# Kernel optimization log

Measured on AMD Instinct MI355X. Metric: run time of the kernel, lower is better.

Reference implementation:

```python
import jax, jax.numpy as jnp
import numpy as np
import math

D_MODEL = 512
NUM_HEADS = 8
D_HEAD = D_MODEL // NUM_HEADS
B, S = 8, 1024


def _rel_shift(pos_score):
    # pos_score: [B, H, S, S] -> Transformer-XL relative shift
    b, h, s1, s2 = pos_score.shape
    padded = jnp.concatenate([jnp.zeros((b, h, s1, 1), pos_score.dtype), pos_score], axis=-1)
    padded = padded.reshape(b, h, s2 + 1, s1)
    return padded[:, :, 1:].reshape(b, h, s1, s2)


def setup_inputs() -> dict:
    key = jax.random.key(0)
    ks = jax.random.split(key, 16)
    scale = 1.0 / math.sqrt(D_MODEL)
    inp = {
        'query': jax.random.normal(ks[0], (B, S, D_MODEL), jnp.float32),
        'key': jax.random.normal(ks[1], (B, S, D_MODEL), jnp.float32),
        'value': jax.random.normal(ks[2], (B, S, D_MODEL), jnp.float32),
        'position_emb': jax.random.normal(ks[3], (B, S, D_MODEL), jnp.float32),
        'Wq': jax.random.normal(ks[4], (D_MODEL, D_MODEL), jnp.float32) * scale,
        'bq': jnp.zeros((D_MODEL,), jnp.float32),
        'Wk': jax.random.normal(ks[5], (D_MODEL, D_MODEL), jnp.float32) * scale,
        'bk': jnp.zeros((D_MODEL,), jnp.float32),
        'Wv': jax.random.normal(ks[6], (D_MODEL, D_MODEL), jnp.float32) * scale,
        'bv': jnp.zeros((D_MODEL,), jnp.float32),
        'Wp': jax.random.normal(ks[7], (D_MODEL, D_MODEL), jnp.float32) * scale,
        'u_bias': jax.random.normal(ks[8], (NUM_HEADS, D_HEAD), jnp.float32) * 0.1,
        'v_bias': jax.random.normal(ks[9], (NUM_HEADS, D_HEAD), jnp.float32) * 0.1,
        'Wo': jax.random.normal(ks[10], (D_MODEL, D_MODEL), jnp.float32) * scale,
        'bo': jnp.zeros((D_MODEL,), jnp.float32),
    }
    return inp


def reference(query, key, value, position_emb, Wq, bq, Wk, bk, Wv, bv, Wp, u_bias, v_bias, Wo, bo):
    b, s, _ = query.shape
    q = (query @ Wq + bq).reshape(b, s, NUM_HEADS, D_HEAD)       # [B,S,H,Dh]
    k = (key @ Wk + bk).reshape(b, s, NUM_HEADS, D_HEAD)
    v = (value @ Wv + bv).reshape(b, s, NUM_HEADS, D_HEAD)
    p = (position_emb @ Wp).reshape(b, s, NUM_HEADS, D_HEAD)
    # content score: (q + u) k^T ; pos score: (q + v) p^T with relative shift
    content_score = jnp.einsum('bqhd,bkhd->bhqk', q + u_bias, k)
    pos_score = _rel_shift(jnp.einsum('bqhd,bkhd->bhqk', q + v_bias, p))
    score = (content_score + pos_score) / math.sqrt(D_MODEL)
    atten = jax.nn.softmax(score, axis=-1)                        # dropout off (eval)
    context = jnp.einsum('bhqk,bkhd->bqhd', atten, v).reshape(b, s, D_MODEL)
    return context @ Wo + bo
```

## Files before the change

### kernel.cpp

```cpp
#include <hip/hip_runtime.h>
#include <cstdint>

typedef unsigned short ushort_t;
typedef __attribute__((ext_vector_type(8))) short bf16x8;
typedef __attribute__((ext_vector_type(4))) float f32x4;

#define S_LEN 1024
#define DHEAD 64

__device__ inline ushort_t f2bf(float f) {
    union { float f; uint32_t u; } c; c.f = f;
    uint32_t u = c.u;
    uint32_t r = u + 0x7FFFu + ((u >> 16) & 1u);
    return (ushort_t)(r >> 16);
}
__device__ inline float bf2f(ushort_t h) {
    union { uint32_t u; float f; } c; c.u = ((uint32_t)h) << 16;
    return c.f;
}
__device__ inline bf16x8 load8(const ushort_t* p) {
    union { uint4 u; bf16x8 v; } c;
    c.u = *reinterpret_cast<const uint4*>(p);
    return c.v;
}

__global__ __launch_bounds__(256) void prep_kernel(
    const float* __restrict__ wq, const float* __restrict__ wk,
    const float* __restrict__ wv, const float* __restrict__ wp,
    const float* __restrict__ wo, ushort_t* __restrict__ ws) {
    __shared__ float tile[64][65];
    int wi = blockIdx.z;
    const float* src = wi == 0 ? wq : wi == 1 ? wk : wi == 2 ? wv : wi == 3 ? wp : wo;
    int cx = blockIdx.x * 64;
    int ry = blockIdx.y * 64;
    int t = threadIdx.x;
    int tr = t >> 4;
    int tc = (t & 15) * 4;
#pragma unroll
    for (int i = 0; i < 4; i++) {
        int r = tr + i * 16;
        float4 f = *reinterpret_cast<const float4*>(src + (size_t)(ry + r) * 512 + cx + tc);
        tile[r][tc] = f.x; tile[r][tc + 1] = f.y; tile[r][tc + 2] = f.z; tile[r][tc + 3] = f.w;
    }
    __syncthreads();
    ushort_t* dst = ws + (size_t)wi * 262144;
#pragma unroll
    for (int i = 0; i < 4; i++) {
        int r = tr + i * 16;
        ushort4 o;
        o.x = f2bf(tile[tc][r]); o.y = f2bf(tile[tc + 1][r]);
        o.z = f2bf(tile[tc + 2][r]); o.w = f2bf(tile[tc + 3][r]);
        *reinterpret_cast<ushort4*>(dst + (size_t)(cx + r) * 512 + ry + tc) = o;
    }
}

__global__ __launch_bounds__(256) void proj_gemm(
    const float* __restrict__ qa, const float* __restrict__ ka,
    const float* __restrict__ va, const float* __restrict__ pa,
    const ushort_t* __restrict__ wT,
    const float* __restrict__ bq, const float* __restrict__ bk,
    const float* __restrict__ bv,
    const float* __restrict__ ub, const float* __restrict__ vb,
    ushort_t* __restrict__ Qu, ushort_t* __restrict__ Qv,
    ushort_t* __restrict__ Kp, ushort_t* __restrict__ Pp,
    ushort_t* __restrict__ Vt) {
    __shared__ ushort_t smem[2][128][72];
    int z = blockIdx.z;
    const float* A = z == 0 ? qa : z == 1 ? ka : z == 2 ? pa : va;
    const ushort_t* Bt = wT + (z == 0 ? 0 : z == 1 ? 262144 : z == 2 ? 786432 : 524288);
    const float* bias = z == 0 ? bq : z == 1 ? bk : z == 3 ? bv : nullptr;

    int tid = threadIdx.x;
    int wid = tid >> 6, lane = tid & 63, quad = lane >> 4, l16 = lane & 15;
    int wr = wid >> 1, wc = wid & 1;
    int row0 = blockIdx.y * 128, col0 = blockIdx.x * 128;

    f32x4 acc[4][4];
#pragma unroll
    for (int i = 0; i < 4; i++)
#pragma unroll
        for (int j = 0; j < 4; j++) acc[i][j] = (f32x4){0.f, 0.f, 0.f, 0.f};

    for (int k0 = 0; k0 < 512; k0 += 64) {
#pragma unroll
        for (int i = 0; i < 4; i++) {
            int cid = tid + i * 256;
            int r = cid >> 3, c8 = cid & 7;
            const float* ap = A + (size_t)(row0 + r) * 512 + k0 + c8 * 8;
            float4 f0 = *reinterpret_cast<const float4*>(ap);
            float4 f1 = *reinterpret_cast<const float4*>(ap + 4);
            union { ushort_t s[8]; uint4 u; } pk;
            pk.s[0] = f2bf(f0.x); pk.s[1] = f2bf(f0.y); pk.s[2] = f2bf(f0.z); pk.s[3] = f2bf(f0.w);
            pk.s[4] = f2bf(f1.x); pk.s[5] = f2bf(f1.y); pk.s[6] = f2bf(f1.z); pk.s[7] = f2bf(f1.w);
            *reinterpret_cast<uint4*>(&smem[0][r][c8 * 8]) = pk.u;
            *reinterpret_cast<uint4*>(&smem[1][r][c8 * 8]) =
                *reinterpret_cast<const uint4*>(Bt + (size_t)(col0 + r) * 512 + k0 + c8 * 8);
        }
        __syncthreads();
#pragma unroll
        for (int kc = 0; kc < 2; kc++) {
            bf16x8 af[4], bg[4];
#pragma unroll
            for (int m = 0; m < 4; m++)
                af[m] = load8(&smem[0][wr * 64 + m * 16 + l16][kc * 32 + quad * 8]);
#pragma unroll
            for (int n = 0; n < 4; n++)
                bg[n] = load8(&smem[1][wc * 64 + n * 16 + l16][kc * 32 + quad * 8]);
#pragma unroll
            for (int m = 0; m < 4; m++)
#pragma unroll
                for (int n = 0; n < 4; n++)
                    acc[m][n] = __builtin_amdgcn_mfma_f32_16x16x32_bf16(af[m], bg[n], acc[m][n], 0, 0, 0);
        }
        __syncthreads();
    }

    if (z == 3) {
        ushort_t (*Ts)[130] = reinterpret_cast<ushort_t(*)[130]>(&smem[0][0][0]);
#pragma unroll
        for (int m = 0; m < 4; m++)
#pragma unroll
            for (int n = 0; n < 4; n++) {
                int dl = wc * 64 + n * 16 + l16;
                float bcol = bv[col0 + dl];
#pragma unroll
                for (int r = 0; r < 4; r++) {
                    int sl = wr * 64 + m * 16 + quad * 4 + r;
                    Ts[dl][sl] = f2bf(acc[m][n][r] + bcol);
                }
            }
        __syncthreads();
        int b_ = row0 >> 10, s0 = row0 & 1023;
#pragma unroll
        for (int p = 0; p < 8; p++) {
            int dl = p * 16 + (tid >> 4);
            int sl = (tid & 15) * 8;
            int col = col0 + dl, h_ = col >> 6, d_ = col & 63;
            ushort_t* dst = Vt + (((size_t)(b_ * 8 + h_)) * 64 + d_) * 1024 + s0 + sl;
            union { uint4 u; ushort_t s[8]; } pk;
#pragma unroll
            for (int e = 0; e < 8; e++) pk.s[e] = Ts[dl][sl + e];
            *reinterpret_cast<uint4*>(dst) = pk.u;
        }
    } else {
#pragma unroll
        for (int m = 0; m < 4; m++)
#pragma unroll
            for (int n = 0; n < 4; n++) {
                int col = col0 + wc * 64 + n * 16 + l16;
                float bcol = bias ? bias[col] : 0.f;
#pragma unroll
                for (int r = 0; r < 4; r++) {
                    int row = row0 + wr * 64 + m * 16 + quad * 4 + r;
                    float val = acc[m][n][r] + bcol;
                    int b_ = row >> 10, s_ = row & 1023, h_ = col >> 6, d_ = col & 63;
                    size_t idx = (((size_t)(b_ * 8 + h_)) * 1024 + s_) * 64 + d_;
                    if (z == 0) {
                        Qu[idx] = f2bf(val + ub[col]);
                        Qv[idx] = f2bf(val + vb[col]);
                    } else {
                        (z == 1 ? Kp : Pp)[idx] = f2bf(val);
                    }
                }
            }
    }
}

__global__ __launch_bounds__(256) void out_gemm(
    const ushort_t* __restrict__ A, const ushort_t* __restrict__ Bt,
    const float* __restrict__ bias, float* __restrict__ outf) {
    __shared__ ushort_t As[128][72];
    __shared__ ushort_t Bs[128][72];
    int tid = threadIdx.x;
    int wid = tid >> 6, lane = tid & 63, quad = lane >> 4, l16 = lane & 15;
    int wr = wid >> 1, wc = wid & 1;
    int row0 = blockIdx.y * 128, col0 = blockIdx.x * 128;

    f32x4 acc[4][4];
#pragma unroll
    for (int i = 0; i < 4; i++)
#pragma unroll
        for (int j = 0; j < 4; j++) acc[i][j] = (f32x4){0.f, 0.f, 0.f, 0.f};

    for (int k0 = 0; k0 < 512; k0 += 64) {
#pragma unroll
        for (int i = 0; i < 4; i++) {
            int cid = tid + i * 256;
            int r = cid >> 3, c8 = cid & 7;
            *reinterpret_cast<uint4*>(&As[r][c8 * 8]) =
                *reinterpret_cast<const uint4*>(A + (size_t)(row0 + r) * 512 + k0 + c8 * 8);
            *reinterpret_cast<uint4*>(&Bs[r][c8 * 8]) =
                *reinterpret_cast<const uint4*>(Bt + (size_t)(col0 + r) * 512 + k0 + c8 * 8);
        }
        __syncthreads();
#pragma unroll
        for (int kc = 0; kc < 2; kc++) {
            bf16x8 af[4], bg[4];
#pragma unroll
            for (int m = 0; m < 4; m++)
                af[m] = load8(&As[wr * 64 + m * 16 + l16][kc * 32 + quad * 8]);
#pragma unroll
            for (int n = 0; n < 4; n++)
                bg[n] = load8(&Bs[wc * 64 + n * 16 + l16][kc * 32 + quad * 8]);
#pragma unroll
            for (int m = 0; m < 4; m++)
#pragma unroll
                for (int n = 0; n < 4; n++)
                    acc[m][n] = __builtin_amdgcn_mfma_f32_16x16x32_bf16(af[m], bg[n], acc[m][n], 0, 0, 0);
        }
        __syncthreads();
    }
#pragma unroll
    for (int m = 0; m < 4; m++)
#pragma unroll
        for (int n = 0; n < 4; n++) {
            int col = col0 + wc * 64 + n * 16 + l16;
#pragma unroll
            for (int r = 0; r < 4; r++) {
                int row = row0 + wr * 64 + m * 16 + quad * 4 + r;
                outf[(size_t)row * 512 + col] = acc[m][n][r] + bias[col];
            }
        }
}

__global__ __launch_bounds__(256) void attn_kernel(
    const ushort_t* __restrict__ Qu, const ushort_t* __restrict__ Qv,
    const ushort_t* __restrict__ Kp, const ushort_t* __restrict__ Pp,
    const ushort_t* __restrict__ Vt, ushort_t* __restrict__ ctxb) {
    __shared__ ushort_t sc[32][1032];
    __shared__ float red1[4][32];
    __shared__ float red2[32][8];
    __shared__ float rowinv[32];

    constexpr float SCL = (float)(1.4426950408889634 / 22.627416997969522);

    int bx = blockIdx.x;
    int bh = bx >> 5, q0 = (bx & 31) << 5;
    int tid = threadIdx.x, wid = tid >> 6, lane = tid & 63;
    int quad = lane >> 4, l16 = lane & 15;

    const ushort_t* Qu_b = Qu + (size_t)bh * S_LEN * DHEAD;
    const ushort_t* Qv_b = Qv + (size_t)bh * S_LEN * DHEAD;
    const ushort_t* K_b  = Kp + (size_t)bh * S_LEN * DHEAD;
    const ushort_t* P_b  = Pp + (size_t)bh * S_LEN * DHEAD;
    const ushort_t* V_b  = Vt + (size_t)bh * DHEAD * S_LEN;

    int kw0 = wid << 8, kw1 = kw0 + 256;

    bf16x8 au0[2], au1[2];
#pragma unroll
    for (int kc = 0; kc < 2; kc++) {
        au0[kc] = load8(Qu_b + (size_t)(q0 + l16) * 64 + kc * 32 + quad * 8);
        au1[kc] = load8(Qu_b + (size_t)(q0 + 16 + l16) * 64 + kc * 32 + quad * 8);
    }

    if (lane < 32) {
        int kz = q0 + lane + 1;
        if (kz >= kw0 && kz < kw1) sc[lane][kz] = 0;
    }

#pragma unroll
    for (int mt = 0; mt < 2; mt++) {
        int q0m = q0 + mt * 16;
        bf16x8 av1[2], av2[2];
#pragma unroll
        for (int kc = 0; kc < 2; kc++) {
            av1[kc] = load8(Qv_b + (size_t)(q0m + l16) * 64 + kc * 32 + quad * 8);
            int r2 = q0m + 1 + l16; if (r2 > S_LEN - 1) r2 = S_LEN - 1;
            av2[kc] = load8(Qv_b + (size_t)r2 * 64 + kc * 32 + quad * 8);
        }
        if (kw0 <= q0m + 15) {
            int wlo = (S_LEN - 16) - q0m + kw0;
            int d1 = kw1 - 1 - q0m; if (d1 > 0) d1 = 0;
            int whi = (S_LEN - 1) + d1;
            int pr = wlo + l16; if (pr > S_LEN - 1) pr = S_LEN - 1;
            bf16x8 p0 = load8(P_b + (size_t)pr * 64 + quad * 8);
            bf16x8 p1 = load8(P_b + (size_t)pr * 64 + 32 + quad * 8);
            for (int wt = wlo; wt <= whi; wt += 16) {
                bf16x8 b0 = p0, b1 = p1;
                if (wt + 16 <= whi) {
                    int pn = wt + 16 + l16; if (pn > S_LEN - 1) pn = S_LEN - 1;
                    p0 = load8(P_b + (size_t)pn * 64 + quad * 8);
                    p1 = load8(P_b + (size_t)pn * 64 + 32 + quad * 8);
                }
                f32x4 acc = (f32x4){0.f, 0.f, 0.f, 0.f};
                acc = __builtin_amdgcn_mfma_f32_16x16x32_bf16(av1[0], b0, acc, 0, 0, 0);
                acc = __builtin_amdgcn_mfma_f32_16x16x32_bf16(av1[1], b1, acc, 0, 0, 0);
#pragma unroll
                for (int r = 0; r < 4; r++) {
                    int m = quad * 4 + r, q = q0m + m;
                    int k = wt + l16 - (S_LEN - 1) + q;
                    if (k >= kw0 && k < kw1 && k <= q) sc[mt * 16 + m][k] = f2bf(acc[r]);
                }
            }
        }
        if (kw1 - 1 >= q0m + 2) {
            int wlo2 = kw0 - q0m - 17; if (wlo2 < 0) wlo2 = 0;
            int whi2 = kw1 - 3 - q0m;
            int pr = wlo2 + l16; if (pr > S_LEN - 1) pr = S_LEN - 1;
            bf16x8 p0 = load8(P_b + (size_t)pr * 64 + quad * 8);
            bf16x8 p1 = load8(P_b + (size_t)pr * 64 + 32 + quad * 8);
            for (int wt = wlo2; wt <= whi2; wt += 16) {
                bf16x8 b0 = p0, b1 = p1;
                if (wt + 16 <= whi2) {
                    int pn = wt + 16 + l16; if (pn > S_LEN - 1) pn = S_LEN - 1;
                    p0 = load8(P_b + (size_t)pn * 64 + quad * 8);
                    p1 = load8(P_b + (size_t)pn * 64 + 32 + quad * 8);
                }
                f32x4 acc = (f32x4){0.f, 0.f, 0.f, 0.f};
                acc = __builtin_amdgcn_mfma_f32_16x16x32_bf16(av2[0], b0, acc, 0, 0, 0);
                acc = __builtin_amdgcn_mfma_f32_16x16x32_bf16(av2[1], b1, acc, 0, 0, 0);
#pragma unroll
                for (int r = 0; r < 4; r++) {
                    int m = quad * 4 + r, q = q0m + m;
                    int k = wt + l16 + q + 2;
                    if (k >= kw0 && k < kw1) sc[mt * 16 + m][k] = f2bf(acc[r]);
                }
            }
        }
    }

    float pm0[4] = {-1e30f, -1e30f, -1e30f, -1e30f};
    float pm1[4] = {-1e30f, -1e30f, -1e30f, -1e30f};
    const ushort_t* Kw = K_b + (size_t)kw0 * 64;
    bf16x8 k0 = load8(Kw + (size_t)l16 * 64 + quad * 8);
    bf16x8 k1 = load8(Kw + (size_t)l16 * 64 + 32 + quad * 8);
    for (int nt = 0; nt < 16; ++nt) {
        int kt = kw0 + nt * 16;
        bf16x8 b0 = k0, b1 = k1;
        if (nt < 15) {
            const ushort_t* kp = Kw + (size_t)((nt + 1) * 16 + l16) * 64;
            k0 = load8(kp + quad * 8);
            k1 = load8(kp + 32 + quad * 8);
        }
        f32x4 a0, a1;
#pragma unroll
        for (int r = 0; r < 4; r++) {
            a0[r] = bf2f(sc[quad * 4 + r][kt + l16]);
            a1[r] = bf2f(sc[16 + quad * 4 + r][kt + l16]);
        }
        a0 = __builtin_amdgcn_mfma_f32_16x16x32_bf16(au0[0], b0, a0, 0, 0, 0);
        a0 = __builtin_amdgcn_mfma_f32_16x16x32_bf16(au0[1], b1, a0, 0, 0, 0);
        a1 = __builtin_amdgcn_mfma_f32_16x16x32_bf16(au1[0], b0, a1, 0, 0, 0);
        a1 = __builtin_amdgcn_mfma_f32_16x16x32_bf16(au1[1], b1, a1, 0, 0, 0);
#pragma unroll
        for (int r = 0; r < 4; r++) {
            sc[quad * 4 + r][kt + l16] = f2bf(a0[r]);
            sc[16 + quad * 4 + r][kt + l16] = f2bf(a1[r]);
            pm0[r] = fmaxf(pm0[r], a0[r]);
            pm1[r] = fmaxf(pm1[r], a1[r]);
        }
    }
#pragma unroll
    for (int off = 1; off < 16; off <<= 1)
#pragma unroll
        for (int r = 0; r < 4; r++) {
            pm0[r] = fmaxf(pm0[r], __shfl_xor(pm0[r], off));
            pm1[r] = fmaxf(pm1[r], __shfl_xor(pm1[r], off));
        }
    if (l16 == 0) {
#pragma unroll
        for (int r = 0; r < 4; r++) {
            red1[wid][quad * 4 + r] = pm0[r];
            red1[wid][16 + quad * 4 + r] = pm1[r];
        }
    }
    __syncthreads();

    int row = tid & 31, cb = tid >> 5;
    float rm = fmaxf(fmaxf(red1[0][row], red1[1][row]), fmaxf(red1[2][row], red1[3][row]));
    float ssum = 0.f;
    ushort_t* sp = &sc[row][cb * 128];
#pragma unroll
    for (int j = 0; j < 16; j++) {
        union { uint4 u; ushort_t s[8]; } in, out;
        in.u = *reinterpret_cast<uint4*>(sp + j * 8);
#pragma unroll
        for (int e = 0; e < 8; e++) {
            float ev = exp2f((bf2f(in.s[e]) - rm) * SCL);
            out.s[e] = f2bf(ev);
            ssum += ev;
        }
        *reinterpret_cast<uint4*>(sp + j * 8) = out.u;
    }
    red2[row][cb] = ssum;
    __syncthreads();
    if (tid < 32) {
        float s = 0.f;
#pragma unroll
        for (int c = 0; c < 8; c++) s += red2[tid][c];
        rowinv[tid] = 1.0f / s;
    }

    int d0 = wid << 4;
    const ushort_t* Vw = V_b + (size_t)(d0 + l16) * 1024;
    bf16x8 vb0 = load8(Vw + quad * 8);
    f32x4 ac0 = (f32x4){0.f, 0.f, 0.f, 0.f};
    f32x4 ac1 = (f32x4){0.f, 0.f, 0.f, 0.f};
    for (int kc = 0; kc < 32; ++kc) {
        bf16x8 b = vb0;
        if (kc < 31) vb0 = load8(Vw + (kc + 1) * 32 + quad * 8);
        bf16x8 a0 = load8(&sc[l16][kc * 32 + quad * 8]);
        bf16x8 a1 = load8(&sc[16 + l16][kc * 32 + quad * 8]);
        ac0 = __builtin_amdgcn_mfma_f32_16x16x32_bf16(a0, b, ac0, 0, 0, 0);
        ac1 = __builtin_amdgcn_mfma_f32_16x16x32_bf16(a1, b, ac1, 0, 0, 0);
    }
    __syncthreads();
    int b_ = bh >> 3, h_ = bh & 7;
#pragma unroll
    for (int r = 0; r < 4; r++) {
        int m = quad * 4 + r;
        ctxb[((size_t)b_ * 1024 + (q0 + m)) * 512 + h_ * 64 + d0 + l16] =
            f2bf(ac0[r] * rowinv[m]);
        ctxb[((size_t)b_ * 1024 + (q0 + 16 + m)) * 512 + h_ * 64 + d0 + l16] =
            f2bf(ac1[r] * rowinv[16 + m]);
    }
}

extern "C" void kernel_launch(void* const* d_in, const int* in_sizes, int n_in,
                              void* d_out, int out_size, void* d_ws, size_t ws_size,
                              hipStream_t stream) {
    const float* q  = (const float*)d_in[0];
    const float* k  = (const float*)d_in[1];
    const float* v  = (const float*)d_in[2];
    const float* pe = (const float*)d_in[3];
    const float* Wq = (const float*)d_in[4];
    const float* bq = (const float*)d_in[5];
    const float* Wk = (const float*)d_in[6];
    const float* bk = (const float*)d_in[7];
    const float* Wv = (const float*)d_in[8];
    const float* bv = (const float*)d_in[9];
    const float* Wp = (const float*)d_in[10];
    const float* ub = (const float*)d_in[11];
    const float* vbias = (const float*)d_in[12];
    const float* Wo = (const float*)d_in[13];
    const float* bo = (const float*)d_in[14];
    float* out = (float*)d_out;
    ushort_t* ws = (ushort_t*)d_ws;

    ushort_t* wT  = ws;
    ushort_t* Qu  = ws + 1310720;
    ushort_t* Qv  = Qu + 4194304;
    ushort_t* Kp  = Qv + 4194304;
    ushort_t* Pp  = Kp + 4194304;
    ushort_t* Vt  = Pp + 4194304;
    ushort_t* ctx = Vt + 4194304;

    prep_kernel<<<dim3(8, 8, 5), 256, 0, stream>>>(Wq, Wk, Wv, Wp, Wo, wT);
    proj_gemm<<<dim3(4, 64, 4), 256, 0, stream>>>(q, k, v, pe, wT, bq, bk, bv,
                                                  ub, vbias, Qu, Qv, Kp, Pp, Vt);
    attn_kernel<<<2048, 256, 0, stream>>>(Qu, Qv, Kp, Pp, Vt, ctx);
    out_gemm<<<dim3(4, 64), 256, 0, stream>>>(ctx, wT + 4 * 262144, bo, out);
}
```

Measured before the change: 337.4 us.

## Pre-convert activations to bf16, retile output GEMM, and deepen prefetch in attention

Adds a prep_act kernel that converts the four fp32 activation tensors to bf16 once. When workspace is large enough, the projection GEMM then loads bf16 tiles directly instead of converting inside the tile loop. Separately, the output GEMM is retiled to 128x64 blocks so twice as many blocks launch, and the attention kernel hoists Qv/K/V fragment loads, uses double-depth register prefetch, and factors the positional-score passes into a helper with a fast unmasked store path. These trade an extra pass over the activations and more register pressure for cheaper GEMM inner loops and better latency hiding.

```diff
diff --git a/kernel.cpp b/kernel.cpp
--- a/kernel.cpp
+++ b/kernel.cpp
@@ -24,18 +24,16 @@
     return c.v;
 }
 
-__global__ __launch_bounds__(256) void prep_kernel(
+__global__ __launch_bounds__(256) void prep_w(
     const float* __restrict__ wq, const float* __restrict__ wk,
     const float* __restrict__ wv, const float* __restrict__ wp,
     const float* __restrict__ wo, ushort_t* __restrict__ ws) {
     __shared__ float tile[64][65];
     int wi = blockIdx.z;
     const float* src = wi == 0 ? wq : wi == 1 ? wk : wi == 2 ? wv : wi == 3 ? wp : wo;
-    int cx = blockIdx.x * 64;
-    int ry = blockIdx.y * 64;
+    int cx = blockIdx.x * 64, ry = blockIdx.y * 64;
     int t = threadIdx.x;
-    int tr = t >> 4;
-    int tc = (t & 15) * 4;
+    int tr = t >> 4, tc = (t & 15) * 4;
 #pragma unroll
     for (int i = 0; i < 4; i++) {
         int r = tr + i * 16;
@@ -54,9 +52,25 @@
     }
 }
 
+__global__ __launch_bounds__(256) void prep_act(
+    const float* __restrict__ q, const float* __restrict__ k,
+    const float* __restrict__ v, const float* __restrict__ p,
+    ushort_t* __restrict__ actb) {
+    int t = blockIdx.x * 256 + threadIdx.x;
+    int sec = blockIdx.y;
+    const float* src = sec == 0 ? q : sec == 1 ? k : sec == 2 ? v : p;
+    ushort_t* dst = actb + (size_t)sec * 4194304;
+    float4 f = reinterpret_cast<const float4*>(src)[t];
+    ushort4 o;
+    o.x = f2bf(f.x); o.y = f2bf(f.y); o.z = f2bf(f.z); o.w = f2bf(f.w);
+    *reinterpret_cast<ushort4*>(dst + (size_t)t * 4) = o;
+}
+
+template<int CVT>
 __global__ __launch_bounds__(256) void proj_gemm(
     const float* __restrict__ qa, const float* __restrict__ ka,
     const float* __restrict__ va, const float* __restrict__ pa,
+    const ushort_t* __restrict__ actb,
     const ushort_t* __restrict__ wT,
     const float* __restrict__ bq, const float* __restrict__ bk,
     const float* __restrict__ bv,
@@ -66,7 +80,8 @@
     ushort_t* __restrict__ Vt) {
     __shared__ ushort_t smem[2][128][72];
     int z = blockIdx.z;
-    const float* A = z == 0 ? qa : z == 1 ? ka : z == 2 ? pa : va;
+    const float* Af = z == 0 ? qa : z == 1 ? ka : z == 2 ? pa : va;
+    const ushort_t* Ab = actb + (size_t)(z == 0 ? 0 : z == 1 ? 1 : z == 2 ? 3 : 2) * 4194304;
     const ushort_t* Bt = wT + (z == 0 ? 0 : z == 1 ? 262144 : z == 2 ? 786432 : 524288);
     const float* bias = z == 0 ? bq : z == 1 ? bk : z == 3 ? bv : nullptr;
 
@@ -86,13 +101,18 @@
         for (int i = 0; i < 4; i++) {
             int cid = tid + i * 256;
             int r = cid >> 3, c8 = cid & 7;
-            const float* ap = A + (size_t)(row0 + r) * 512 + k0 + c8 * 8;
-            float4 f0 = *reinterpret_cast<const float4*>(ap);
-            float4 f1 = *reinterpret_cast<const float4*>(ap + 4);
-            union { ushort_t s[8]; uint4 u; } pk;
-            pk.s[0] = f2bf(f0.x); pk.s[1] = f2bf(f0.y); pk.s[2] = f2bf(f0.z); pk.s[3] = f2bf(f0.w);
-            pk.s[4] = f2bf(f1.x); pk.s[5] = f2bf(f1.y); pk.s[6] = f2bf(f1.z); pk.s[7] = f2bf(f1.w);
-            *reinterpret_cast<uint4*>(&smem[0][r][c8 * 8]) = pk.u;
+            if (CVT) {
+                const float* ap = Af + (size_t)(row0 + r) * 512 + k0 + c8 * 8;
+                float4 f0 = *reinterpret_cast<const float4*>(ap);
+                float4 f1 = *reinterpret_cast<const float4*>(ap + 4);
+                union { ushort_t s[8]; uint4 u; } pk;
+                pk.s[0] = f2bf(f0.x); pk.s[1] = f2bf(f0.y); pk.s[2] = f2bf(f0.z); pk.s[3] = f2bf(f0.w);
+                pk.s[4] = f2bf(f1.x); pk.s[5] = f2bf(f1.y); pk.s[6] = f2bf(f1.z); pk.s[7] = f2bf(f1.w);
+                *reinterpret_cast<uint4*>(&smem[0][r][c8 * 8]) = pk.u;
+            } else {
+                *reinterpret_cast<uint4*>(&smem[0][r][c8 * 8]) =
+                    *reinterpret_cast<const uint4*>(Ab + (size_t)(row0 + r) * 512 + k0 + c8 * 8);
+            }
             *reinterpret_cast<uint4*>(&smem[1][r][c8 * 8]) =
                 *reinterpret_cast<const uint4*>(Bt + (size_t)(col0 + r) * 512 + k0 + c8 * 8);
         }
@@ -170,15 +190,14 @@
     const ushort_t* __restrict__ A, const ushort_t* __restrict__ Bt,
     const float* __restrict__ bias, float* __restrict__ outf) {
     __shared__ ushort_t As[128][72];
-    __shared__ ushort_t Bs[128][72];
+    __shared__ ushort_t Bs[64][72];
     int tid = threadIdx.x;
     int wid = tid >> 6, lane = tid & 63, quad = lane >> 4, l16 = lane & 15;
-    int wr = wid >> 1, wc = wid & 1;
-    int row0 = blockIdx.y * 128, col0 = blockIdx.x * 128;
-
-    f32x4 acc[4][4];
-#pragma unroll
-    for (int i = 0; i < 4; i++)
+    int row0 = blockIdx.y * 128, col0 = blockIdx.x * 64;
+
+    f32x4 acc[2][4];
+#pragma unroll
+    for (int i = 0; i < 2; i++)
 #pragma unroll
         for (int j = 0; j < 4; j++) acc[i][j] = (f32x4){0.f, 0.f, 0.f, 0.f};
 
@@ -189,21 +208,26 @@
             int r = cid >> 3, c8 = cid & 7;
             *reinterpret_cast<uint4*>(&As[r][c8 * 8]) =
                 *reinterpret_cast<const uint4*>(A + (size_t)(row0 + r) * 512 + k0 + c8 * 8);
+        }
+#pragma unroll
+        for (int i = 0; i < 2; i++) {
+            int cid = tid + i * 256;
+            int r = cid >> 3, c8 = cid & 7;
             *reinterpret_cast<uint4*>(&Bs[r][c8 * 8]) =
                 *reinterpret_cast<const uint4*>(Bt + (size_t)(col0 + r) * 512 + k0 + c8 * 8);
         }
         __syncthreads();
 #pragma unroll
         for (int kc = 0; kc < 2; kc++) {
-            bf16x8 af[4], bg[4];
-#pragma unroll
-            for (int m = 0; m < 4; m++)
-                af[m] = load8(&As[wr * 64 + m * 16 + l16][kc * 32 + quad * 8]);
+            bf16x8 af[2], bg[4];
+#pragma unroll
+            for (int m = 0; m < 2; m++)
+                af[m] = load8(&As[wid * 32 + m * 16 + l16][kc * 32 + quad * 8]);
 #pragma unroll
             for (int n = 0; n < 4; n++)
-                bg[n] = load8(&Bs[wc * 64 + n * 16 + l16][kc * 32 + quad * 8]);
-#pragma unroll
-            for (int m = 0; m < 4; m++)
+                bg[n] = load8(&Bs[n * 16 + l16][kc * 32 + quad * 8]);
+#pragma unroll
+            for (int m = 0; m < 2; m++)
 #pragma unroll
                 for (int n = 0; n < 4; n++)
                     acc[m][n] = __builtin_amdgcn_mfma_f32_16x16x32_bf16(af[m], bg[n], acc[m][n], 0, 0, 0);
@@ -211,16 +235,62 @@
         __syncthreads();
     }
 #pragma unroll
-    for (int m = 0; m < 4; m++)
+    for (int m = 0; m < 2; m++)
 #pragma unroll
         for (int n = 0; n < 4; n++) {
-            int col = col0 + wc * 64 + n * 16 + l16;
+            int col = col0 + n * 16 + l16;
 #pragma unroll
             for (int r = 0; r < 4; r++) {
-                int row = row0 + wr * 64 + m * 16 + quad * 4 + r;
+                int row = row0 + wid * 32 + m * 16 + quad * 4 + r;
                 outf[(size_t)row * 512 + col] = acc[m][n][r] + bias[col];
             }
         }
+}
+
+__device__ __forceinline__ void pos_pass(
+    const ushort_t* __restrict__ P_b, ushort_t (*sc)[1032],
+    const bf16x8* av, int wlo, int whi, int kbb, int collim, int mtrow,
+    int kw0, int kw1, int quad, int l16) {
+    if (whi < wlo) return;
+    int nw = (whi - wlo) / 16 + 1;
+    bf16x8 pb0[2], pb1[2];
+#pragma unroll
+    for (int i = 0; i < 2; i++) {
+        if (i < nw) {
+            int pr = wlo + i * 16 + l16; if (pr > S_LEN - 1) pr = S_LEN - 1;
+            pb0[i] = load8(P_b + (size_t)pr * 64 + quad * 8);
+            pb1[i] = load8(P_b + (size_t)pr * 64 + 32 + quad * 8);
+        }
+    }
+    for (int w = 0; w < nw; w++) {
+        int cur = w & 1;
+        bf16x8 b0 = pb0[cur], b1 = pb1[cur];
+        if (w + 2 < nw) {
+            int pr = wlo + (w + 2) * 16 + l16; if (pr > S_LEN - 1) pr = S_LEN - 1;
+            pb0[cur] = load8(P_b + (size_t)pr * 64 + quad * 8);
+            pb1[cur] = load8(P_b + (size_t)pr * 64 + 32 + quad * 8);
+        }
+        f32x4 acc = (f32x4){0.f, 0.f, 0.f, 0.f};
+        acc = __builtin_amdgcn_mfma_f32_16x16x32_bf16(av[0], b0, acc, 0, 0, 0);
+        acc = __builtin_amdgcn_mfma_f32_16x16x32_bf16(av[1], b1, acc, 0, 0, 0);
+        int wt = wlo + w * 16;
+        int kb = wt + kbb;
+        if (kb >= kw0 && kb + 30 < kw1 && wt + 15 <= collim) {
+#pragma unroll
+            for (int r = 0; r < 4; r++) {
+                int m = quad * 4 + r;
+                sc[mtrow + m][kb + m + l16] = f2bf(acc[r]);
+            }
+        } else {
+#pragma unroll
+            for (int r = 0; r < 4; r++) {
+                int m = quad * 4 + r;
+                int k = kb + m + l16;
+                if (k >= kw0 && k < kw1 && (wt + l16) <= collim)
+                    sc[mtrow + m][k] = f2bf(acc[r]);
+            }
+        }
+    }
 }
 
 __global__ __launch_bounds__(256) void attn_kernel(
@@ -246,13 +316,32 @@
     const ushort_t* V_b  = Vt + (size_t)bh * DHEAD * S_LEN;
 
     int kw0 = wid << 8, kw1 = kw0 + 256;
-
-    bf16x8 au0[2], au1[2];
+    int d0 = wid << 4;
+
+    bf16x8 au0[2], au1[2], av1[2][2], av2[2][2];
 #pragma unroll
     for (int kc = 0; kc < 2; kc++) {
         au0[kc] = load8(Qu_b + (size_t)(q0 + l16) * 64 + kc * 32 + quad * 8);
         au1[kc] = load8(Qu_b + (size_t)(q0 + 16 + l16) * 64 + kc * 32 + quad * 8);
-    }
+#pragma unroll
+        for (int mt = 0; mt < 2; mt++) {
+            int q0m = q0 + mt * 16;
+            av1[mt][kc] = load8(Qv_b + (size_t)(q0m + l16) * 64 + kc * 32 + quad * 8);
+            int r2 = q0m + 1 + l16; if (r2 > S_LEN - 1) r2 = S_LEN - 1;
+            av2[mt][kc] = load8(Qv_b + (size_t)r2 * 64 + kc * 32 + quad * 8);
+        }
+    }
+    const ushort_t* Kw = K_b + (size_t)kw0 * 64;
+    bf16x8 kb0[2], kb1[2];
+#pragma unroll
+    for (int i = 0; i < 2; i++) {
+        kb0[i] = load8(Kw + (size_t)(i * 16 + l16) * 64 + quad * 8);
+        kb1[i] = load8(Kw + (size_t)(i * 16 + l16) * 64 + 32 + quad * 8);
+    }
+    const ushort_t* Vw = V_b + (size_t)(d0 + l16) * 1024;
+    bf16x8 vv[2];
+    vv[0] = load8(Vw + quad * 8);
+    vv[1] = load8(Vw + 32 + quad * 8);
 
     if (lane < 32) {
         int kz = q0 + lane + 1;
@@ -262,77 +351,28 @@
 #pragma unroll
     for (int mt = 0; mt < 2; mt++) {
         int q0m = q0 + mt * 16;
-        bf16x8 av1[2], av2[2];
-#pragma unroll
-        for (int kc = 0; kc < 2; kc++) {
-            av1[kc] = load8(Qv_b + (size_t)(q0m + l16) * 64 + kc * 32 + quad * 8);
-            int r2 = q0m + 1 + l16; if (r2 > S_LEN - 1) r2 = S_LEN - 1;
-            av2[kc] = load8(Qv_b + (size_t)r2 * 64 + kc * 32 + quad * 8);
-        }
-        if (kw0 <= q0m + 15) {
-            int wlo = (S_LEN - 16) - q0m + kw0;
-            int d1 = kw1 - 1 - q0m; if (d1 > 0) d1 = 0;
-            int whi = (S_LEN - 1) + d1;
-            int pr = wlo + l16; if (pr > S_LEN - 1) pr = S_LEN - 1;
-            bf16x8 p0 = load8(P_b + (size_t)pr * 64 + quad * 8);
-            bf16x8 p1 = load8(P_b + (size_t)pr * 64 + 32 + quad * 8);
-            for (int wt = wlo; wt <= whi; wt += 16) {
-                bf16x8 b0 = p0, b1 = p1;
-                if (wt + 16 <= whi) {
-                    int pn = wt + 16 + l16; if (pn > S_LEN - 1) pn = S_LEN - 1;
-                    p0 = load8(P_b + (size_t)pn * 64 + quad * 8);
-                    p1 = load8(P_b + (size_t)pn * 64 + 32 + quad * 8);
-                }
-                f32x4 acc = (f32x4){0.f, 0.f, 0.f, 0.f};
-                acc = __builtin_amdgcn_mfma_f32_16x16x32_bf16(av1[0], b0, acc, 0, 0, 0);
-                acc = __builtin_amdgcn_mfma_f32_16x16x32_bf16(av1[1], b1, acc, 0, 0, 0);
-#pragma unroll
-                for (int r = 0; r < 4; r++) {
-                    int m = quad * 4 + r, q = q0m + m;
-                    int k = wt + l16 - (S_LEN - 1) + q;
-                    if (k >= kw0 && k < kw1 && k <= q) sc[mt * 16 + m][k] = f2bf(acc[r]);
-                }
-            }
-        }
-        if (kw1 - 1 >= q0m + 2) {
-            int wlo2 = kw0 - q0m - 17; if (wlo2 < 0) wlo2 = 0;
-            int whi2 = kw1 - 3 - q0m;
-            int pr = wlo2 + l16; if (pr > S_LEN - 1) pr = S_LEN - 1;
-            bf16x8 p0 = load8(P_b + (size_t)pr * 64 + quad * 8);
-            bf16x8 p1 = load8(P_b + (size_t)pr * 64 + 32 + quad * 8);
-            for (int wt = wlo2; wt <= whi2; wt += 16) {
-                bf16x8 b0 = p0, b1 = p1;
-                if (wt + 16 <= whi2) {
-                    int pn = wt + 16 + l16; if (pn > S_LEN - 1) pn = S_LEN - 1;
-                    p0 = load8(P_b + (size_t)pn * 64 + quad * 8);
-                    p1 = load8(P_b + (size_t)pn * 64 + 32 + quad * 8);
-                }
-                f32x4 acc = (f32x4){0.f, 0.f, 0.f, 0.f};
-                acc = __builtin_amdgcn_mfma_f32_16x16x32_bf16(av2[0], b0, acc, 0, 0, 0);
-                acc = __builtin_amdgcn_mfma_f32_16x16x32_bf16(av2[1], b1, acc, 0, 0, 0);
-#pragma unroll
-                for (int r = 0; r < 4; r++) {
-                    int m = quad * 4 + r, q = q0m + m;
-                    int k = wt + l16 + q + 2;
-                    if (k >= kw0 && k < kw1) sc[mt * 16 + m][k] = f2bf(acc[r]);
-                }
-            }
-        }
+        int wlo = (S_LEN - 16) - q0m + kw0;
+        int d1 = kw1 - 1 - q0m; if (d1 > 0) d1 = 0;
+        int whi = (S_LEN - 1) + d1;
+        pos_pass(P_b, sc, av1[mt], wlo, whi, q0m - (S_LEN - 1), S_LEN - 1,
+                 mt * 16, kw0, kw1, quad, l16);
+        int wlo2 = kw0 - q0m - 17; if (wlo2 < 0) wlo2 = 0;
+        int whi2 = kw1 - 3 - q0m;
+        pos_pass(P_b, sc, av2[mt], wlo2, whi2, q0m + 2, 1 << 30,
+                 mt * 16, kw0, kw1, quad, l16);
     }
 
     float pm0[4] = {-1e30f, -1e30f, -1e30f, -1e30f};
     float pm1[4] = {-1e30f, -1e30f, -1e30f, -1e30f};
-    const ushort_t* Kw = K_b + (size_t)kw0 * 64;
-    bf16x8 k0 = load8(Kw + (size_t)l16 * 64 + quad * 8);
-    bf16x8 k1 = load8(Kw + (size_t)l16 * 64 + 32 + quad * 8);
     for (int nt = 0; nt < 16; ++nt) {
+        int cur = nt & 1;
+        bf16x8 b0 = kb0[cur], b1 = kb1[cur];
+        if (nt + 2 < 16) {
+            const ushort_t* kp = Kw + (size_t)((nt + 2) * 16 + l16) * 64;
+            kb0[cur] = load8(kp + quad * 8);
+            kb1[cur] = load8(kp + 32 + quad * 8);
+        }
         int kt = kw0 + nt * 16;
-        bf16x8 b0 = k0, b1 = k1;
-        if (nt < 15) {
-            const ushort_t* kp = Kw + (size_t)((nt + 1) * 16 + l16) * 64;
-            k0 = load8(kp + quad * 8);
-            k1 = load8(kp + 32 + quad * 8);
-        }
         f32x4 a0, a1;
 #pragma unroll
         for (int r = 0; r < 4; r++) {
@@ -392,14 +432,11 @@
         rowinv[tid] = 1.0f / s;
     }
 
-    int d0 = wid << 4;
-    const ushort_t* Vw = V_b + (size_t)(d0 + l16) * 1024;
-    bf16x8 vb0 = load8(Vw + quad * 8);
     f32x4 ac0 = (f32x4){0.f, 0.f, 0.f, 0.f};
     f32x4 ac1 = (f32x4){0.f, 0.f, 0.f, 0.f};
     for (int kc = 0; kc < 32; ++kc) {
-        bf16x8 b = vb0;
-        if (kc < 31) vb0 = load8(Vw + (kc + 1) * 32 + quad * 8);
+        bf16x8 b = vv[kc & 1];
+        if (kc + 2 < 32) vv[kc & 1] = load8(Vw + (kc + 2) * 32 + quad * 8);
         bf16x8 a0 = load8(&sc[l16][kc * 32 + quad * 8]);
         bf16x8 a1 = load8(&sc[16 + l16][kc * 32 + quad * 8]);
         ac0 = __builtin_amdgcn_mfma_f32_16x16x32_bf16(a0, b, ac0, 0, 0, 0);
@@ -444,11 +481,24 @@
     ushort_t* Kp  = Qv + 4194304;
     ushort_t* Pp  = Kp + 4194304;
     ushort_t* Vt  = Pp + 4194304;
-    ushort_t* ctx = Vt + 4194304;
-
-    prep_kernel<<<dim3(8, 8, 5), 256, 0, stream>>>(Wq, Wk, Wv, Wp, Wo, wT);
-    proj_gemm<<<dim3(4, 64, 4), 256, 0, stream>>>(q, k, v, pe, wT, bq, bk, bv,
-                                                  ub, vbias, Qu, Qv, Kp, Pp, Vt);
-    attn_kernel<<<2048, 256, 0, stream>>>(Qu, Qv, Kp, Pp, Vt, ctx);
-    out_gemm<<<dim3(4, 64), 256, 0, stream>>>(ctx, wT + 4 * 262144, bo, out);
-}
+    ushort_t* actb = Vt + 4194304;
+    ushort_t* ctx_big = actb;
+
+    const size_t need_big = (size_t)(1310720 + 9 * 4194304) * 2;
+    bool big = ws_size >= need_big;
+
+    prep_w<<<dim3(8, 8, 5), 256, 0, stream>>>(Wq, Wk, Wv, Wp, Wo, wT);
+    if (big) {
+        prep_act<<<dim3(4096, 4), 256, 0, stream>>>(q, k, v, pe, actb);
+        proj_gemm<0><<<dim3(4, 64, 4), 256, 0, stream>>>(q, k, v, pe, actb, wT,
+            bq, bk, bv, ub, vbias, Qu, Qv, Kp, Pp, Vt);
+        attn_kernel<<<2048, 256, 0, stream>>>(Qu, Qv, Kp, Pp, Vt, ctx_big);
+        out_gemm<<<dim3(8, 64), 256, 0, stream>>>(ctx_big, wT + 4 * 262144, bo, out);
+    } else {
+        ushort_t* ctx = actb;
+        proj_gemm<1><<<dim3(4, 64, 4), 256, 0, stream>>>(q, k, v, pe, nullptr, wT,
+            bq, bk, bv, ub, vbias, Qu, Qv, Kp, Pp, Vt);
+        attn_kernel<<<2048, 256, 0, stream>>>(Qu, Qv, Kp, Pp, Vt, ctx);
+        out_gemm<<<dim3(8, 64), 256, 0, stream>>>(ctx, wT + 4 * 262144, bo, out);
+    }
+}
```

Result: slower. 791.1 us (+134.5%).
